# Performance work log

Measured on AMD Instinct MI355X. Metric: run time of the kernel, lower is better.

Reference implementation:

```python
import jax, jax.numpy as jnp
import numpy as np


def setup_inputs() -> dict:
    key = jax.random.key(0)
    k1, k2 = jax.random.split(key)
    return {
        "embeddings": jax.random.normal(k1, (4, 768, 32, 32), dtype=jnp.float32),
        "database": jax.random.normal(k2, (20000, 768), dtype=jnp.float32),
        "k": 3,
        "out_h": 512,
        "out_w": 512,
    }


def reference(embeddings, database, k, out_h, out_w):
    # embeddings: [B, D, h, w]  (segmenter hidden state), database: [N, D]
    B, D, h, w = embeddings.shape
    # B x h x w x D -> B x (h*w) x D query layout, as in _get_ood_scores
    q = jnp.transpose(embeddings, (0, 2, 3, 1)).reshape(B, h * w, D)
    # squared Euclidean distances via (||q||^2 + ||x||^2 - 2 q.x)
    q2 = jnp.sum(q * q, axis=-1)[..., None]                 # [B, hw, 1]
    x2 = jnp.sum(database * database, axis=-1)[None, None]  # [1, 1, N]
    d2 = q2 + x2 - 2.0 * jnp.einsum("bqd,nd->bqn", q, database)
    dist = jnp.sqrt(jnp.maximum(d2, 1e-12))                 # [B, hw, N]
    # k smallest distances (sklearn kneighbors) then mean over neighbors
    neg_topk, _ = jax.lax.top_k(-dist, k)                   # [B, hw, k]
    ood = jnp.mean(-neg_topk, axis=-1).reshape(B, h, w)
    # F.interpolate(..., mode='bilinear', align_corners=False) == half-pixel bilinear
    ood_up = jax.image.resize(ood[:, None], (B, 1, out_h, out_w), method="bilinear")
    return ood_up
```

## Files before the change

kernel.cpp:

```cpp
#include <hip/hip_runtime.h>
#include <hip/hip_bf16.h>
#include <math.h>

constexpr int B    = 4;
constexpr int D    = 768;
constexpr int HW   = 1024;
constexpr int M    = B * HW;
constexpr int NDB  = 20000;
constexpr int LT   = 158;
constexpr int OUTH = 512;
constexpr int OUTW = 512;

constexpr int BM     = 256;
constexpr int BN     = 128;
constexpr int KSTEPS = D / 64;
constexpr int NSPLIT = 16;
constexpr int NT2    = 79;
constexpr int STEPB  = 128 * 64;

typedef int   i32x8  __attribute__((ext_vector_type(8)));
typedef float f32x16 __attribute__((ext_vector_type(16)));

__device__ __forceinline__ void insert3(float& t0, float& t1, float& t2, float d) {
    float a0 = fminf(d, t0);
    float b0 = fmaxf(d, t0);
    float a1 = fminf(b0, t1);
    float b1 = fmaxf(b0, t1);
    t0 = a0; t1 = a1;
    t2 = fminf(b1, t2);
}

__device__ __forceinline__ unsigned int pack4_fp8(float a, float b, float c, float d) {
    int v = __builtin_amdgcn_cvt_pk_fp8_f32(a, b, 0, false);
    v = __builtin_amdgcn_cvt_pk_fp8_f32(c, d, v, true);
    return (unsigned int)v;
}

__device__ __forceinline__ void gl_lds16(const unsigned char* g, unsigned char* l) {
    __builtin_amdgcn_global_load_lds(
        (const __attribute__((address_space(1))) void*)g,
        (__attribute__((address_space(3))) void*)l, 16, 0, 0);
}

__global__ __launch_bounds__(256) void convert_all(const float* __restrict__ db,
                                                   const float* __restrict__ emb,
                                                   uint4* __restrict__ dbt8,
                                                   uint4* __restrict__ qbt8,
                                                   float* __restrict__ x2p,
                                                   float* __restrict__ q2p) {
    __shared__ float panel[128][68];
    __shared__ float part[512];
    const int g = blockIdx.y;
    const int t = threadIdx.x;

    if (blockIdx.x < LT) {
        const int lt = blockIdx.x;
        const int n0 = lt * 128;

        #pragma unroll
        for (int pass = 0; pass < 8; ++pass) {
            int idx = pass * 256 + t;
            int row = idx >> 4, c4 = idx & 15;
            int n = n0 + row;
            float4 v = make_float4(0.f, 0.f, 0.f, 0.f);
            if (n < NDB) v = *(const float4*)(db + (size_t)n * D + g * 64 + c4 * 4);
            *(float4*)&panel[row][c4 * 4] = v;
        }
        __syncthreads();
        #pragma unroll
        for (int pass = 0; pass < 2; ++pass) {
            int idx = pass * 256 + t;
            int r  = idx & 31;
            int kc = (idx >> 5) & 1;
            int h2 = (idx >> 6) & 1;
            int rg = idx >> 7;
            int row  = rg * 32 + r;
            int kloc = kc * 32 + h2 * 16;
            float4 va = *(const float4*)&panel[row][kloc + 0];
            float4 vb = *(const float4*)&panel[row][kloc + 4];
            float4 vc = *(const float4*)&panel[row][kloc + 8];
            float4 vd = *(const float4*)&panel[row][kloc + 12];
            float ss = va.x*va.x + va.y*va.y + va.z*va.z + va.w*va.w
                     + vb.x*vb.x + vb.y*vb.y + vb.z*vb.z + vb.w*vb.w
                     + vc.x*vc.x + vc.y*vc.y + vc.z*vc.z + vc.w*vc.w
                     + vd.x*vd.x + vd.y*vd.y + vd.z*vd.z + vd.w*vd.w;
            uint4 o;
            o.x = pack4_fp8(va.x, va.y, va.z, va.w);
            o.y = pack4_fp8(vb.x, vb.y, vb.z, vb.w);
            o.z = pack4_fp8(vc.x, vc.y, vc.z, vc.w);
            o.w = pack4_fp8(vd.x, vd.y, vd.z, vd.w);
            dbt8[((size_t)lt * KSTEPS + g) * 512 + idx] = o;
            part[idx] = ss;
        }
        __syncthreads();
        if (t < 128) {
            int base = (t >> 5) * 128 + (t & 31);
            float s = part[base] + part[base + 32] + part[base + 64] + part[base + 96];
            x2p[((size_t)lt * KSTEPS + g) * 128 + t] = s;
        }
    } else {
        const int qt = blockIdx.x - LT;
        const int b  = qt >> 3;
        const int p0 = (qt & 7) * 128;

        #pragma unroll
        for (int pass = 0; pass < 2; ++pass) {
            int idx = pass * 256 + t;
            int r  = idx & 31;
            int kc = (idx >> 5) & 1;
            int h2 = (idx >> 6) & 1;
            int rg = idx >> 7;
            int prow = rg * 32 + r;
            int kb = g * 64 + kc * 32 + h2 * 16;
            const float* src = emb + ((size_t)b * D + kb) * HW + p0 + prow;
            float v[16];
            float ss = 0.f;
            #pragma unroll
            for (int j = 0; j < 16; ++j) {
                v[j] = src[(size_t)j * HW];
                ss = fmaf(v[j], v[j], ss);
            }
            uint4 o;
            o.x = pack4_fp8(-2.f*v[0],  -2.f*v[1],  -2.f*v[2],  -2.f*v[3]);
            o.y = pack4_fp8(-2.f*v[4],  -2.f*v[5],  -2.f*v[6],  -2.f*v[7]);
            o.z = pack4_fp8(-2.f*v[8],  -2.f*v[9],  -2.f*v[10], -2.f*v[11]);
            o.w = pack4_fp8(-2.f*v[12], -2.f*v[13], -2.f*v[14], -2.f*v[15]);
            qbt8[((size_t)qt * KSTEPS + g) * 512 + idx] = o;
            part[idx] = ss;
        }
        __syncthreads();
        if (t < 128) {
            int base = (t >> 5) * 128 + (t & 31);
            float s = part[base] + part[base + 32] + part[base + 64] + part[base + 96];
            q2p[((size_t)qt * KSTEPS + g) * 128 + t] = s;
        }
    }
}

__global__ __launch_bounds__(256, 2) void gemm_topk(const unsigned char* __restrict__ dbt8,
                                                    const unsigned char* __restrict__ qbt8,
                                                    const float* __restrict__ x2p,
                                                    float* __restrict__ partials) {
    __shared__ __align__(16) unsigned char Bsm[2 * 8192];
    __shared__ float red[4][BN][3];

    const int tid  = threadIdx.x;
    const int lane = tid & 63;
    const int w    = tid >> 6;
    const int lts  = w >> 1;
    const int wr   = w & 1;
    const int h    = lane >> 5;
    const int l31  = lane & 31;

    const int bid   = blockIdx.x;
    const int xcd   = bid & 7;
    const int j     = bid >> 3;
    const int sp    = xcd + 8 * (j >> 5);
    const int qtile = j & 31;
    const int m0    = qtile * BN;

    int b_off[4];
    #pragma unroll
    for (int j4 = 0; j4 < 4; ++j4) b_off[j4] = j4 * 2048 + h * 512 + l31 * 16;

    const unsigned char* aT = dbt8 + (size_t)(2 * sp + lts) * KSTEPS * STEPB
                              + wr * 4096 + h * 512 + l31 * 16;

    const unsigned char* bQ = qbt8 + (size_t)qtile * KSTEPS * STEPB + w * 2048 + lane * 16;
    unsigned char* bD = Bsm + w * 2048;

    auto ldA = [&](i32x8& x0, i32x8& x1, const unsigned char* p) {
        int4 a = *(const int4*)(p);
        int4 b = *(const int4*)(p + 1024);
        int4 c = *(const int4*)(p + 2048);
        int4 d = *(const int4*)(p + 3072);
        x0 = (i32x8){a.x, a.y, a.z, a.w, b.x, b.y, b.z, b.w};
        x1 = (i32x8){c.x, c.y, c.z, c.w, d.x, d.y, d.z, d.w};
    };
    auto ldB = [&](i32x8& f, const unsigned char* Bb, int off) {
        int4 lo = *(const int4*)(Bb + off);
        int4 hi = *(const int4*)(Bb + off + 1024);
        f = (i32x8){lo.x, lo.y, lo.z, lo.w, hi.x, hi.y, hi.z, hi.w};
    };

    gl_lds16(bQ,        bD);
    gl_lds16(bQ + 1024, bD + 1024);

    float t0[4], t1[4], t2[4];
    #pragma unroll
    for (int j4 = 0; j4 < 4; ++j4) { t0[j4] = INFINITY; t1[j4] = INFINITY; t2[j4] = INFINITY; }

    for (int tile = sp; tile < NT2; tile += NSPLIT) {
        const bool lastTile = (tile + NSPLIT >= NT2);

        float sx = 1e30f;
        {
            int n = tile * BM + w * 64 + lane;
            if (n < NDB) {
                const float* p = x2p + (size_t)(n >> 7) * (KSTEPS * 128) + (n & 127);
                sx = 0.f;
                #pragma unroll
                for (int g = 0; g < KSTEPS; ++g) sx += p[g * 128];
            }
        }

        f32x16 acc[2][4];
        #pragma unroll
        for (int i = 0; i < 2; ++i)
            #pragma unroll
            for (int j4 = 0; j4 < 4; ++j4)
                #pragma unroll
                for (int r = 0; r < 16; ++r) acc[i][j4][r] = 0.f;

        i32x8 af0, af1, an0, an1;
        ldA(af0, af1, aT);

        #pragma unroll 2
        for (int g = 0; g < KSTEPS; ++g) {
            __syncthreads();

            if (g + 1 < KSTEPS) {
                gl_lds16(bQ + (g + 1) * STEPB,        bD + ((g + 1) & 1) * 8192);
                gl_lds16(bQ + (g + 1) * STEPB + 1024, bD + ((g + 1) & 1) * 8192 + 1024);
            } else if (!lastTile) {
                gl_lds16(bQ,        bD);
                gl_lds16(bQ + 1024, bD + 1024);
            }

            if (g + 1 < KSTEPS) ldA(an0, an1, aT + (g + 1) * STEPB);

            const unsigned char* Bb = Bsm + (g & 1) * 8192;
            i32x8 bf[4];
            #pragma unroll
            for (int j4 = 0; j4 < 4; ++j4) ldB(bf[j4], Bb, b_off[j4]);

            #pragma unroll
            for (int j4 = 0; j4 < 4; ++j4) {
                acc[0][j4] = __builtin_amdgcn_mfma_scale_f32_32x32x64_f8f6f4(
                    af0, bf[j4], acc[0][j4], 0, 0, 0, 0x7f7f7f7f, 0, 0x7f7f7f7f);
                acc[1][j4] = __builtin_amdgcn_mfma_scale_f32_32x32x64_f8f6f4(
                    af1, bf[j4], acc[1][j4], 0, 0, 0, 0x7f7f7f7f, 0, 0x7f7f7f7f);
            }
            af0 = an0; af1 = an1;
        }
        aT += (size_t)2 * NSPLIT * KSTEPS * STEPB;

        #pragma unroll
        for (int i = 0; i < 2; ++i) {
            #pragma unroll
            for (int rg2 = 0; rg2 < 4; ++rg2) {
                #pragma unroll
                for (int rr = 0; rr < 4; ++rr) {
                    float xv = __shfl(sx, i * 32 + rg2 * 8 + 4 * h + rr);
                    #pragma unroll
                    for (int j4 = 0; j4 < 4; ++j4)
                        insert3(t0[j4], t1[j4], t2[j4], acc[i][j4][rg2 * 4 + rr] + xv);
                }
            }
        }
    }

    #pragma unroll
    for (int j4 = 0; j4 < 4; ++j4) {
        float o0 = __shfl_xor(t0[j4], 32);
        float o1 = __shfl_xor(t1[j4], 32);
        float o2 = __shfl_xor(t2[j4], 32);
        insert3(t0[j4], t1[j4], t2[j4], o0);
        insert3(t0[j4], t1[j4], t2[j4], o1);
        insert3(t0[j4], t1[j4], t2[j4], o2);
    }
    if (h == 0) {
        #pragma unroll
        for (int j4 = 0; j4 < 4; ++j4) {
            int col = j4 * 32 + l31;
            red[w][col][0] = t0[j4];
            red[w][col][1] = t1[j4];
            red[w][col][2] = t2[j4];
        }
    }
    __syncthreads();
    if (tid < BN) {
        float a0 = red[0][tid][0], a1 = red[0][tid][1], a2 = red[0][tid][2];
        #pragma unroll
        for (int ww = 1; ww < 4; ++ww) {
            insert3(a0, a1, a2, red[ww][tid][0]);
            insert3(a0, a1, a2, red[ww][tid][1]);
            insert3(a0, a1, a2, red[ww][tid][2]);
        }
        float* dst = partials + ((size_t)(m0 + tid) * NSPLIT + sp) * 3;
        dst[0] = a0; dst[1] = a1; dst[2] = a2;
    }
}

__global__ __launch_bounds__(256) void merge_ood(const float* __restrict__ partials,
                                                 const float* __restrict__ q2p,
                                                 float* __restrict__ ood) {
    int m = blockIdx.x * 256 + threadIdx.x;
    if (m >= M) return;
    const float* pp = partials + (size_t)m * NSPLIT * 3;
    float a0 = INFINITY, a1 = INFINITY, a2 = INFINITY;
    #pragma unroll
    for (int j = 0; j < NSPLIT * 3; ++j) insert3(a0, a1, a2, pp[j]);
    const float* qp = q2p + (size_t)(m >> 7) * KSTEPS * 128 + (m & 127);
    float q = 0.f;
    #pragma unroll
    for (int g = 0; g < KSTEPS; ++g) q += qp[g * 128];
    float d0 = sqrtf(fmaxf(q + a0, 1e-12f));
    float d1 = sqrtf(fmaxf(q + a1, 1e-12f));
    float d2 = sqrtf(fmaxf(q + a2, 1e-12f));
    ood[m] = (d0 + d1 + d2) * (1.f / 3.f);
}

__global__ __launch_bounds__(256) void upsample(const float* __restrict__ ood,
                                                float* __restrict__ out) {
    int idx = blockIdx.x * 256 + threadIdx.x;
    int ox = idx & (OUTW - 1);
    int oy = (idx >> 9) & (OUTH - 1);
    int bb = idx >> 18;
    float sx = (ox + 0.5f) * (32.f / OUTW) - 0.5f;
    float sy = (oy + 0.5f) * (32.f / OUTH) - 0.5f;
    float fx = floorf(sx), fy = floorf(sy);
    float wx = sx - fx, wy = sy - fy;
    int x0 = max(0, min(31, (int)fx));
    int x1 = max(0, min(31, (int)fx + 1));
    int y0 = max(0, min(31, (int)fy));
    int y1 = max(0, min(31, (int)fy + 1));
    const float* src = ood + bb * 1024;
    float v00 = src[y0 * 32 + x0];
    float v01 = src[y0 * 32 + x1];
    float v10 = src[y1 * 32 + x0];
    float v11 = src[y1 * 32 + x1];
    float top = v00 + wx * (v01 - v00);
    float bot = v10 + wx * (v11 - v10);
    out[idx] = top + wy * (bot - top);
}

extern "C" void kernel_launch(void* const* d_in, const int* in_sizes, int n_in,
                              void* d_out, int out_size, void* d_ws, size_t ws_size,
                              hipStream_t stream) {
    const float* emb = (const float*)d_in[0];
    const float* db  = (const float*)d_in[1];
    float* out = (float*)d_out;

    char* ws = (char*)d_ws;
    unsigned char* dbt8 = (unsigned char*)ws;
    unsigned char* qbt8 = (unsigned char*)(ws + 15532032);
    float* x2p      = (float*)(ws + 18677760);
    float* q2p      = (float*)(ws + 19648512);
    float* ood      = (float*)(ws + 19845120);
    float* partials = (float*)(ws + 19861504);

    convert_all<<<dim3(LT + 32, KSTEPS), 256, 0, stream>>>(db, emb, (uint4*)dbt8,
                                                           (uint4*)qbt8, x2p, q2p);
    gemm_topk<<<NSPLIT * 32, 256, 0, stream>>>(dbt8, qbt8, x2p, partials);
    merge_ood<<<(M + 255) / 256, 256, 0, stream>>>(partials, q2p, ood);
    upsample<<<(B * OUTH * OUTW) / 256, 256, 0, stream>>>(ood, out);
}
```

Before: 182.5 us.

## Deepen query LDS pipeline to four buffers with prefetch distance two

Grows the shared-memory buffer for the query operand from two stages to four. Global-to-LDS loads are now issued two k-steps ahead, and the block-wide barrier runs only every other k-step. It also loads the A and B MFMA fragments directly into vector halves instead of building them from temporaries, and raises the k-loop unroll to 4. The aim is to hide global-load latency and cut barrier overhead, at the price of twice the LDS and possible correctness risk if async-load completion is not awaited before reads that no longer sit behind a barrier.

```diff
diff --git a/kernel.cpp b/kernel.cpp
--- a/kernel.cpp
+++ b/kernel.cpp
@@ -141,7 +141,7 @@
                                                     const unsigned char* __restrict__ qbt8,
                                                     const float* __restrict__ x2p,
                                                     float* __restrict__ partials) {
-    __shared__ __align__(16) unsigned char Bsm[2 * 8192];
+    __shared__ __align__(16) unsigned char Bsm[4 * 8192];
     __shared__ float red[4][BN][3];
 
     const int tid  = threadIdx.x;
@@ -170,21 +170,20 @@
     unsigned char* bD = Bsm + w * 2048;
 
     auto ldA = [&](i32x8& x0, i32x8& x1, const unsigned char* p) {
-        int4 a = *(const int4*)(p);
-        int4 b = *(const int4*)(p + 1024);
-        int4 c = *(const int4*)(p + 2048);
-        int4 d = *(const int4*)(p + 3072);
-        x0 = (i32x8){a.x, a.y, a.z, a.w, b.x, b.y, b.z, b.w};
-        x1 = (i32x8){c.x, c.y, c.z, c.w, d.x, d.y, d.z, d.w};
+        *(int4*)&x0       = *(const int4*)(p);
+        *((int4*)&x0 + 1) = *(const int4*)(p + 1024);
+        *(int4*)&x1       = *(const int4*)(p + 2048);
+        *((int4*)&x1 + 1) = *(const int4*)(p + 3072);
     };
     auto ldB = [&](i32x8& f, const unsigned char* Bb, int off) {
-        int4 lo = *(const int4*)(Bb + off);
-        int4 hi = *(const int4*)(Bb + off + 1024);
-        f = (i32x8){lo.x, lo.y, lo.z, lo.w, hi.x, hi.y, hi.z, hi.w};
+        *(int4*)&f       = *(const int4*)(Bb + off);
+        *((int4*)&f + 1) = *(const int4*)(Bb + off + 1024);
     };
 
-    gl_lds16(bQ,        bD);
-    gl_lds16(bQ + 1024, bD + 1024);
+    gl_lds16(bQ,                bD);
+    gl_lds16(bQ + 1024,         bD + 1024);
+    gl_lds16(bQ + STEPB,        bD + 8192);
+    gl_lds16(bQ + STEPB + 1024, bD + 8192 + 1024);
 
     float t0[4], t1[4], t2[4];
     #pragma unroll
@@ -215,21 +214,25 @@
         i32x8 af0, af1, an0, an1;
         ldA(af0, af1, aT);
 
-        #pragma unroll 2
+        #pragma unroll 4
         for (int g = 0; g < KSTEPS; ++g) {
-            __syncthreads();
-
-            if (g + 1 < KSTEPS) {
-                gl_lds16(bQ + (g + 1) * STEPB,        bD + ((g + 1) & 1) * 8192);
-                gl_lds16(bQ + (g + 1) * STEPB + 1024, bD + ((g + 1) & 1) * 8192 + 1024);
-            } else if (!lastTile) {
-                gl_lds16(bQ,        bD);
-                gl_lds16(bQ + 1024, bD + 1024);
+            if ((g & 1) == 0) __syncthreads();
+
+            {
+                int gs = g + 2;
+                unsigned char* dst = bD + ((g + 2) & 3) * 8192;
+                if (gs < KSTEPS) {
+                    gl_lds16(bQ + gs * STEPB,        dst);
+                    gl_lds16(bQ + gs * STEPB + 1024, dst + 1024);
+                } else if (!lastTile) {
+                    gl_lds16(bQ + (gs - KSTEPS) * STEPB,        dst);
+                    gl_lds16(bQ + (gs - KSTEPS) * STEPB + 1024, dst + 1024);
+                }
             }
 
             if (g + 1 < KSTEPS) ldA(an0, an1, aT + (g + 1) * STEPB);
 
-            const unsigned char* Bb = Bsm + (g & 1) * 8192;
+            const unsigned char* Bb = Bsm + (g & 3) * 8192;
             i32x8 bf[4];
             #pragma unroll
             for (int j4 = 0; j4 < 4; ++j4) ldB(bf[j4], Bb, b_off[j4]);
```

After: 303.9 us. +66.5%, slower.
